# Kernel tuning notes

Hardware: AMD Instinct MI355X
Metric: run time of the kernel (lower is better)

The kernel has to match this reference:

```python
import jax, jax.numpy as jnp
import numpy as np

D_VOC, P_VOC, M_VOC = 2048, 1024, 4096
H = 256
T = 32
LD, LP, LM = 24, 12, 20


def _norm_adj(key, n):
    # binary graph + self loops, row-normalized (matches GCN.normalize(adj+I))
    a = (jax.random.uniform(key, (n, n)) < 0.002).astype(jnp.float32)
    a = a + jnp.eye(n, dtype=jnp.float32)
    rs = a.sum(axis=1)
    rinv = jnp.where(rs > 0, 1.0 / rs, 0.0)
    return rinv[:, None] * a


def setup_inputs() -> dict:
    key = jax.random.key(0)
    ks = jax.random.split(key, 32)
    s = float(1.0 / np.sqrt(H))
    u = lambda k, shape, sc: jax.random.uniform(k, shape, minval=-sc, maxval=sc, dtype=jnp.float32)
    inp = {
        'diag_codes': jax.random.randint(ks[0], (T, LD), 0, D_VOC),
        'proc_codes': jax.random.randint(ks[1], (T, LP), 0, P_VOC),
        'med_codes': jax.random.randint(ks[2], (T - 1, LM), 0, M_VOC),
        'diag_emb': u(ks[3], (D_VOC, H), 0.1),
        'proc_emb': u(ks[4], (P_VOC, H), 0.1),
        'gru_d_wih': u(ks[5], (3 * H, H), s), 'gru_d_whh': u(ks[6], (3 * H, H), s),
        'gru_d_bih': u(ks[7], (3 * H,), s), 'gru_d_bhh': u(ks[8], (3 * H,), s),
        'gru_p_wih': u(ks[9], (3 * H, H), s), 'gru_p_whh': u(ks[10], (3 * H, H), s),
        'gru_p_bih': u(ks[11], (3 * H,), s), 'gru_p_bhh': u(ks[12], (3 * H,), s),
        'q_w': u(ks[13], (2 * H, H), s), 'q_b': u(ks[14], (H,), s),
        'adj_ehr': _norm_adj(ks[15], M_VOC),
        'adj_ddi': _norm_adj(ks[16], M_VOC),
        'w1_ehr': u(ks[17], (M_VOC, H), s), 'b1_ehr': u(ks[18], (H,), s),
        'w2_ehr': u(ks[19], (H, H), s), 'b2_ehr': u(ks[20], (H,), s),
        'w1_ddi': u(ks[21], (M_VOC, H), s), 'b1_ddi': u(ks[22], (H,), s),
        'w2_ddi': u(ks[23], (H, H), s), 'b2_ddi': u(ks[24], (H,), s),
        'inter': jax.random.normal(ks[25], (1,), dtype=jnp.float32) / H,
        'proj_w': u(ks[26], (2 * H, H), s), 'proj_b': u(ks[27], (H,), s),
    }
    return inp


def _gru(x, wih, whh, bih, bhh):
    # torch.nn.GRU cell math; x: [T, H] -> outputs [T, H]
    def step(h, xt):
        gi = xt @ wih.T + bih
        gh = h @ whh.T + bhh
        ir, iz, inn = jnp.split(gi, 3)
        hr, hz, hn = jnp.split(gh, 3)
        r = jax.nn.sigmoid(ir + hr)
        z = jax.nn.sigmoid(iz + hz)
        n = jnp.tanh(inn + r * hn)
        h2 = (1.0 - z) * n + z * h
        return h2, h2
    _, ys = jax.lax.scan(step, jnp.zeros((x.shape[-1],), x.dtype), x)
    return ys


def _gcn(adj, w1, b1, w2, b2):
    # input features are identity, so first support mm(I, w1) == w1
    h1 = jax.nn.relu(adj @ w1 + b1)
    return adj @ (h1 @ w2) + b2


def reference(diag_codes, proc_codes, med_codes, diag_emb, proc_emb,
              gru_d_wih, gru_d_whh, gru_d_bih, gru_d_bhh,
              gru_p_wih, gru_p_whh, gru_p_bih, gru_p_bhh,
              q_w, q_b, adj_ehr, adj_ddi,
              w1_ehr, b1_ehr, w2_ehr, b2_ehr,
              w1_ddi, b1_ddi, w2_ddi, b2_ddi,
              inter, proj_w, proj_b):
    # ---- PatientEncoder: gather + sum codes per visit, GRU over visits ----
    seq_d = diag_emb[diag_codes].sum(axis=1)            # [T, H]
    seq_p = proc_emb[proc_codes].sum(axis=1)            # [T, H]
    od = _gru(seq_d, gru_d_wih, gru_d_whh, gru_d_bih, gru_d_bhh)
    op = _gru(seq_p, gru_p_wih, gru_p_whh, gru_p_bih, gru_p_bhh)
    feats = jnp.concatenate([od, op], axis=-1)          # [T, 2H]
    queries = jax.nn.relu(feats) @ q_w + q_b            # [T, H] (Sequential(ReLU, Linear))
    query = queries[-1:]                                # [1, H]
    history_keys = queries[:-1]                         # [T-1, H]
    # multi-hot history medication values (scatter)
    tm1 = med_codes.shape[0]
    history_values = jnp.zeros((tm1, M_VOC), jnp.float32).at[
        jnp.arange(tm1)[:, None], med_codes].set(1.0)   # [T-1, M_VOC]
    # ---- PriorEncoder ----
    prior = _gcn(adj_ehr, w1_ehr, b1_ehr, w2_ehr, b2_ehr) \
        - inter[0] * _gcn(adj_ddi, w1_ddi, b1_ddi, w2_ddi, b2_ddi)  # [M_VOC, H]
    w_emb = jax.nn.softmax(query @ prior.T, axis=-1)    # [1, M_VOC]
    # diag(w) @ prior == broadcast row-scale (the fused gather-weighted-scale)
    gc1 = w_emb.reshape(-1, 1) * prior                  # [M_VOC, H]
    visit_w = jax.nn.softmax(query @ history_keys.T, axis=-1)  # [1, T-1]
    wv = (visit_w @ history_values).reshape(-1, 1)      # [M_VOC, 1]
    gc2 = wv * prior                                    # [M_VOC, H]
    return jnp.concatenate([gc1, gc2], axis=-1) @ proj_w + proj_b  # [M_VOC, H]
```

## Files before the change

kernel.cpp:

```cpp
#include <hip/hip_runtime.h>
#include <hip/hip_bf16.h>

#define HD   256
#define TT   32
#define MV   4096
#define LD_  24
#define LP_  12
#define LM_  20
#define MAXNZ 96
#define SCAN_WPB 12

typedef _Float16 h2v __attribute__((ext_vector_type(2)));
typedef _Float16 h8  __attribute__((ext_vector_type(8)));

__device__ __forceinline__ float fdot2(h2v a, h2v b, float c) {
#if __has_builtin(__builtin_amdgcn_fdot2)
  return __builtin_amdgcn_fdot2(a, b, c, false);
#else
  return c + (float)a[0] * (float)b[0] + (float)a[1] * (float)b[1];
#endif
}

#define PIN2(x) { float _t = __builtin_bit_cast(float, x); \
                  asm volatile("" : "+v"(_t));             \
                  x = __builtin_bit_cast(h2v, _t); }

__global__ __launch_bounds__(768) void k0_cvt(
    const float* __restrict__ whh_d, const float* __restrict__ whh_p,
    h8* __restrict__ wt)
{
  const int i = blockIdx.x, b = blockIdx.y, g = threadIdx.x;
  const float* whh = b ? whh_p : whh_d;
  const float* src = whh + (size_t)g * HD + 8 * i;
  h8 v;
#pragma unroll
  for (int e = 0; e < 8; ++e) v[e] = (_Float16)src[e];
  wt[((size_t)b * 32 + i) * 768 + g] = v;
}

__global__ __launch_bounds__(768) void k1_embed_gi(
    const int* __restrict__ dc, const int* __restrict__ pc,
    const float* __restrict__ demb, const float* __restrict__ pemb,
    const float* __restrict__ wih_d, const float* __restrict__ bih_d,
    const float* __restrict__ wih_p, const float* __restrict__ bih_p,
    float* __restrict__ GI)
{
  const int t = blockIdx.x, b = blockIdx.y;
  const int* codes = b ? pc : dc;
  const int L = b ? LP_ : LD_;
  const float* emb = b ? pemb : demb;
  const float* wih = b ? wih_p : wih_d;
  const float* bih = b ? bih_p : bih_d;
  __shared__ float s[HD];
  const int j = threadIdx.x;
  if (j < HD) {
    float acc = 0.f;
    for (int l = 0; l < L; ++l) acc += emb[(size_t)codes[t * L + l] * HD + j];
    s[j] = acc;
  }
  __syncthreads();
  const int g = j;
  float acc = bih[g];
  const float* wr = wih + (size_t)g * HD;
  for (int k = 0; k < HD; k += 4) {
    float4 w4 = *(const float4*)(wr + k);
    acc = fmaf(w4.x, s[k], acc);
    acc = fmaf(w4.y, s[k + 1], acc);
    acc = fmaf(w4.z, s[k + 2], acc);
    acc = fmaf(w4.w, s[k + 3], acc);
  }
  GI[((size_t)b * TT + t) * 768 + g] = acc;
}

__global__ __launch_bounds__(768)
__attribute__((amdgpu_waves_per_eu(3, 3)))
void k23_fused(
    const float* __restrict__ GI, const h8* __restrict__ wt,
    const float* __restrict__ bhh_d, const float* __restrict__ bhh_p,
    float* __restrict__ feats,
    const float* __restrict__ adj_e, const float* __restrict__ adj_d,
    const float* __restrict__ w1_e, const float* __restrict__ b1_e,
    const float* __restrict__ w1_d, const float* __restrict__ b1_d,
    float* __restrict__ h1, int* __restrict__ cnt_g,
    int* __restrict__ cols_g, float* __restrict__ vals_g)
{
  __shared__ h8 hbuf[2][32];
  __shared__ float ghs[768];
  __shared__ int   scols[SCAN_WPB][MAXNZ];
  __shared__ float svals[SCAN_WPB][MAXNZ];

  if (blockIdx.x < 2) {
    const int b = blockIdx.x, g = threadIdx.x;
    const float* gi = GI + (size_t)b * TT * 768;
    const float* bhh = b ? bhh_p : bhh_d;

    h2v w[128];
    {
      const h8* wrow = wt + (size_t)b * 32 * 768 + g;
#pragma unroll
      for (int i = 0; i < 32; ++i) {
        union { h8 v; h2v p[4]; } u;
        u.v = wrow[(size_t)i * 768];
        w[4 * i + 0] = u.p[0];
        w[4 * i + 1] = u.p[1];
        w[4 * i + 2] = u.p[2];
        w[4 * i + 3] = u.p[3];
      }
    }
#pragma unroll
    for (int i = 0; i < 128; ++i) PIN2(w[i])

    const float bh = bhh[g];
    float hreg = 0.f;
    if (g < HD) ((_Float16*)&hbuf[0][0])[g] = (_Float16)0.f;
    __syncthreads();

    for (int t = 0; t < TT; ++t) {
      const float* git = gi + t * 768;
      float ir = 0.f, iz = 0.f, inn = 0.f;
      if (g < HD) { ir = git[g]; iz = git[HD + g]; inn = git[2 * HD + g]; }

      const h8* hb = hbuf[t & 1];
      float d0 = 0.f, d1 = 0.f, d2 = 0.f, d3 = 0.f;
#pragma unroll
      for (int i = 0; i < 32; ++i) {
        union { h8 v; h2v p[4]; } u;
        u.v = hb[i];
        d0 = fdot2(w[4 * i + 0], u.p[0], d0);
        d1 = fdot2(w[4 * i + 1], u.p[1], d1);
        d2 = fdot2(w[4 * i + 2], u.p[2], d2);
        d3 = fdot2(w[4 * i + 3], u.p[3], d3);
      }
      ghs[g] = (d0 + d1) + (d2 + d3) + bh;
      __syncthreads();
      if (g < HD) {
        const float hr = ghs[g], hz = ghs[HD + g], hn = ghs[2 * HD + g];
        const float r = 1.f / (1.f + __expf(-(ir + hr)));
        const float z = 1.f / (1.f + __expf(-(iz + hz)));
        const float n = tanhf(inn + r * hn);
        hreg = (1.f - z) * n + z * hreg;
        ((_Float16*)&hbuf[(t & 1) ^ 1][0])[g] = (_Float16)hreg;
        feats[(size_t)t * 512 + b * HD + g] = hreg;
      }
      __syncthreads();
    }
    return;
  }

  const int w = threadIdx.x >> 6, lane = threadIdx.x & 63;
  const int rg = (blockIdx.x - 2) * SCAN_WPB + w;
  if (rg >= 2 * MV) return;
  const int bsel = rg >> 12;
  const int r = rg & (MV - 1);
  const float* adj = (bsel ? adj_d : adj_e) + (size_t)r * MV;
  const float* w1 = bsel ? w1_d : w1_e;
  const float* b1 = bsel ? b1_d : b1_e;

  float4 ev[16];
#pragma unroll
  for (int c = 0; c < 16; ++c)
    ev[c] = *(const float4*)(adj + c * 256 + lane * 4);

  int cl = 0;
#pragma unroll
  for (int c = 0; c < 16; ++c)
    cl += (ev[c].x != 0.f) + (ev[c].y != 0.f) + (ev[c].z != 0.f) + (ev[c].w != 0.f);

  int pref = cl;
#pragma unroll
  for (int ofs = 1; ofs < 64; ofs <<= 1) {
    int v = __shfl_up(pref, ofs, 64);
    if (lane >= ofs) pref += v;
  }
  const int total = __shfl(pref, 63, 64);
  int pos = pref - cl;

#pragma unroll
  for (int c = 0; c < 16; ++c) {
    const float vv[4] = {ev[c].x, ev[c].y, ev[c].z, ev[c].w};
#pragma unroll
    for (int e = 0; e < 4; ++e) {
      if (vv[e] != 0.f) {
        if (pos < MAXNZ) {
          scols[w][pos] = c * 256 + lane * 4 + e;
          svals[w][pos] = vv[e];
        }
        ++pos;
      }
    }
  }
  const int n = total > MAXNZ ? MAXNZ : total;

  float4 acc = *(const float4*)(b1 + lane * 4);
  for (int k = 0; k < n; ++k) {
    const int col = scols[w][k];
    const float v = svals[w][k];
    const float4 wv4 = *(const float4*)(w1 + (size_t)col * HD + lane * 4);
    acc.x = fmaf(v, wv4.x, acc.x);
    acc.y = fmaf(v, wv4.y, acc.y);
    acc.z = fmaf(v, wv4.z, acc.z);
    acc.w = fmaf(v, wv4.w, acc.w);
  }
  float4 hro;
  hro.x = fmaxf(acc.x, 0.f); hro.y = fmaxf(acc.y, 0.f);
  hro.z = fmaxf(acc.z, 0.f); hro.w = fmaxf(acc.w, 0.f);
  *(float4*)(h1 + (size_t)rg * HD + lane * 4) = hro;

  if (lane == 0) cnt_g[rg] = n;
  for (int k = lane; k < n; k += 64) {
    cols_g[(size_t)rg * MAXNZ + k] = scols[w][k];
    vals_g[(size_t)rg * MAXNZ + k] = svals[w][k];
  }
}

__global__ __launch_bounds__(256) void k2b_queries(
    const float* __restrict__ feats, const float* __restrict__ q_w,
    const float* __restrict__ q_b, float* __restrict__ queries)
{
  const int t = blockIdx.x, j = threadIdx.x;
  __shared__ float f[512];
  f[j] = fmaxf(feats[(size_t)t * 512 + j], 0.f);
  f[j + 256] = fmaxf(feats[(size_t)t * 512 + 256 + j], 0.f);
  __syncthreads();
  float acc = q_b[j];
  for (int k = 0; k < 512; ++k) acc = fmaf(f[k], q_w[(size_t)k * HD + j], acc);
  queries[(size_t)t * HD + j] = acc;
}

__global__ __launch_bounds__(512) void k4_z(
    const float* __restrict__ h1, const float* __restrict__ w2_e,
    const float* __restrict__ w2_d, float* __restrict__ zz)
{
  const int blk = blockIdx.x, b = blockIdx.y;
  const int t = threadIdx.x;
  const int j = t & 255, half = t >> 8;
  const float* w2 = b ? w2_d : w2_e;
  const float* h1b = h1 + (size_t)b * MV * HD + (size_t)blk * 8 * HD;
  __shared__ float tile[8][HD];
  __shared__ float part[8][HD];
  {
    float4* t4 = (float4*)tile;
    const float4* s4 = (const float4*)h1b;
    t4[t] = s4[t];
  }
  __syncthreads();
  float acc[8];
#pragma unroll
  for (int r = 0; r < 8; ++r) acc[r] = 0.f;
  const int k0 = half * 128;
  for (int k = k0; k < k0 + 128; k += 4) {
    float wa = w2[(size_t)(k + 0) * HD + j];
    float wb = w2[(size_t)(k + 1) * HD + j];
    float wc = w2[(size_t)(k + 2) * HD + j];
    float wd = w2[(size_t)(k + 3) * HD + j];
#pragma unroll
    for (int r = 0; r < 8; ++r) {
      float4 tv = *(const float4*)&tile[r][k];
      acc[r] = fmaf(tv.x, wa, acc[r]);
      acc[r] = fmaf(tv.y, wb, acc[r]);
      acc[r] = fmaf(tv.z, wc, acc[r]);
      acc[r] = fmaf(tv.w, wd, acc[r]);
    }
  }
  if (half == 1) {
#pragma unroll
    for (int r = 0; r < 8; ++r) part[r][j] = acc[r];
  }
  __syncthreads();
  if (half == 0) {
    float* zb = zz + (size_t)b * MV * HD + (size_t)blk * 8 * HD;
#pragma unroll
    for (int r = 0; r < 8; ++r) zb[r * HD + j] = acc[r] + part[r][j];
  }
}

__global__ __launch_bounds__(256) void k5_prior(
    const float* __restrict__ zz, const int* __restrict__ cnt_g,
    const int* __restrict__ cols_g, const float* __restrict__ vals_g,
    const float* __restrict__ b2_e, const float* __restrict__ b2_d,
    const float* __restrict__ inter, const float* __restrict__ queries,
    float* __restrict__ prior, float* __restrict__ s1)
{
  const int r = blockIdx.x, j = threadIdx.x;
  __shared__ float red[256];
  float acc_e = b2_e[j];
  {
    const int ne = cnt_g[r];
    const int* ce = cols_g + (size_t)r * MAXNZ;
    const float* ve = vals_g + (size_t)r * MAXNZ;
    for (int k = 0; k < ne; ++k)
      acc_e = fmaf(ve[k], zz[(size_t)ce[k] * HD + j], acc_e);
  }
  float acc_d = b2_d[j];
  {
    const int nd = cnt_g[MV + r];
    const int* cd = cols_g + (size_t)(MV + r) * MAXNZ;
    const float* vd = vals_g + (size_t)(MV + r) * MAXNZ;
    const float* zd = zz + (size_t)MV * HD;
    for (int k = 0; k < nd; ++k)
      acc_d = fmaf(vd[k], zd[(size_t)cd[k] * HD + j], acc_d);
  }
  const float pr = acc_e - inter[0] * acc_d;
  prior[(size_t)r * HD + j] = pr;
  red[j] = queries[31 * HD + j] * pr;
  __syncthreads();
  for (int s = 128; s > 0; s >>= 1) {
    if (j < s) red[j] += red[j + s];
    __syncthreads();
  }
  if (j == 0) s1[r] = red[0];
}

__global__ __launch_bounds__(1024) void k6a_softmax(
    const float* __restrict__ s1, const float* __restrict__ queries,
    float* __restrict__ w_emb, float* __restrict__ visw)
{
  const int j = threadIdx.x;
  __shared__ float red[1024];
  __shared__ float s2[31];
  float m = -1e30f;
  for (int i = j; i < MV; i += 1024) m = fmaxf(m, s1[i]);
  red[j] = m;
  __syncthreads();
  for (int s = 512; s > 0; s >>= 1) {
    if (j < s) red[j] = fmaxf(red[j], red[j + s]);
    __syncthreads();
  }
  const float mx = red[0];
  __syncthreads();
  float sum = 0.f;
  for (int i = j; i < MV; i += 1024) sum += __expf(s1[i] - mx);
  red[j] = sum;
  __syncthreads();
  for (int s = 512; s > 0; s >>= 1) {
    if (j < s) red[j] += red[j + s];
    __syncthreads();
  }
  const float inv = 1.f / red[0];
  for (int i = j; i < MV; i += 1024) w_emb[i] = __expf(s1[i] - mx) * inv;

  if (j < 31) {
    float acc = 0.f;
    for (int k = 0; k < HD; ++k)
      acc = fmaf(queries[31 * HD + k], queries[(size_t)j * HD + k], acc);
    s2[j] = acc;
  }
  __syncthreads();
  if (j == 0) {
    float mm = -1e30f;
    for (int t = 0; t < 31; ++t) mm = fmaxf(mm, s2[t]);
    float ss = 0.f;
    for (int t = 0; t < 31; ++t) ss += __expf(s2[t] - mm);
    const float is = 1.f / ss;
    for (int t = 0; t < 31; ++t) visw[t] = __expf(s2[t] - mm) * is;
  }
}

__global__ __launch_bounds__(1024) void k6b_wv(
    const int* __restrict__ med, const float* __restrict__ visw,
    float* __restrict__ wv)
{
  __shared__ int mc[31 * LM_];
  __shared__ float vw[31];
  const int j = threadIdx.x;
  if (j < 31 * LM_) mc[j] = med[j];
  if (j < 31) vw[j] = visw[j];
  __syncthreads();
  const int m = blockIdx.x * 1024 + j;
  float acc = 0.f;
  for (int t = 0; t < 31; ++t) {
    bool found = false;
#pragma unroll
    for (int l = 0; l < LM_; ++l) found = found || (mc[t * LM_ + l] == m);
    if (found) acc += vw[t];
  }
  wv[m] = acc;
}

__global__ __launch_bounds__(512) void k7_out(
    const float* __restrict__ prior, const float* __restrict__ w_emb,
    const float* __restrict__ wv, const float* __restrict__ proj_w,
    const float* __restrict__ proj_b, float* __restrict__ out)
{
  const int blk = blockIdx.x;
  const int t = threadIdx.x;
  const int j = t & 255, half = t >> 8;
  const int r0 = blk * 8;
  __shared__ float tile[8][HD];
  __shared__ float part[8][HD];
  __shared__ float we[8], wvv[8];
  {
    float4* t4 = (float4*)tile;
    const float4* s4 = (const float4*)(prior + (size_t)r0 * HD);
    t4[t] = s4[t];
  }
  if (t < 8) { we[t] = w_emb[r0 + t]; wvv[t] = wv[r0 + t]; }
  __syncthreads();
  const float* wmat = proj_w + (size_t)half * HD * HD;
  float acc[8];
#pragma unroll
  for (int r = 0; r < 8; ++r) acc[r] = 0.f;
  for (int k = 0; k < HD; k += 4) {
    float wa = wmat[(size_t)(k + 0) * HD + j];
    float wb = wmat[(size_t)(k + 1) * HD + j];
    float wc = wmat[(size_t)(k + 2) * HD + j];
    float wd = wmat[(size_t)(k + 3) * HD + j];
#pragma unroll
    for (int r = 0; r < 8; ++r) {
      float4 tv = *(const float4*)&tile[r][k];
      acc[r] = fmaf(tv.x, wa, acc[r]);
      acc[r] = fmaf(tv.y, wb, acc[r]);
      acc[r] = fmaf(tv.z, wc, acc[r]);
      acc[r] = fmaf(tv.w, wd, acc[r]);
    }
  }
  if (half == 1) {
#pragma unroll
    for (int r = 0; r < 8; ++r) part[r][j] = acc[r];
  }
  __syncthreads();
  if (half == 0) {
    const float pb = proj_b[j];
#pragma unroll
    for (int r = 0; r < 8; ++r)
      out[(size_t)(r0 + r) * HD + j] = we[r] * acc[r] + wvv[r] * part[r][j] + pb;
  }
}

extern "C" void kernel_launch(void* const* d_in, const int* in_sizes, int n_in,
                              void* d_out, int out_size, void* d_ws, size_t ws_size,
                              hipStream_t stream) {
  const int* diag_codes = (const int*)d_in[0];
  const int* proc_codes = (const int*)d_in[1];
  const int* med_codes  = (const int*)d_in[2];
  const float* diag_emb = (const float*)d_in[3];
  const float* proc_emb = (const float*)d_in[4];
  const float* wih_d = (const float*)d_in[5];
  const float* whh_d = (const float*)d_in[6];
  const float* bih_d = (const float*)d_in[7];
  const float* bhh_d = (const float*)d_in[8];
  const float* wih_p = (const float*)d_in[9];
  const float* whh_p = (const float*)d_in[10];
  const float* bih_p = (const float*)d_in[11];
  const float* bhh_p = (const float*)d_in[12];
  const float* q_w = (const float*)d_in[13];
  const float* q_b = (const float*)d_in[14];
  const float* adj_ehr = (const float*)d_in[15];
  const float* adj_ddi = (const float*)d_in[16];
  const float* w1_ehr = (const float*)d_in[17];
  const float* b1_ehr = (const float*)d_in[18];
  const float* w2_ehr = (const float*)d_in[19];
  const float* b2_ehr = (const float*)d_in[20];
  const float* w1_ddi = (const float*)d_in[21];
  const float* b1_ddi = (const float*)d_in[22];
  const float* w2_ddi = (const float*)d_in[23];
  const float* b2_ddi = (const float*)d_in[24];
  const float* inter = (const float*)d_in[25];
  const float* proj_w = (const float*)d_in[26];
  const float* proj_b = (const float*)d_in[27];
  float* out = (float*)d_out;

  float* ws = (float*)d_ws;
  size_t off = 0;
  float* GI      = ws + off; off += 2 * TT * 768;
  float* feats   = ws + off; off += TT * 512;
  float* queries = ws + off; off += TT * HD;
  float* h1      = ws + off; off += 2 * (size_t)MV * HD;
  float* zz      = ws + off; off += 2 * (size_t)MV * HD;
  float* prior   = ws + off; off += (size_t)MV * HD;
  float* s1      = ws + off; off += MV;
  float* w_emb   = ws + off; off += MV;
  float* visw    = ws + off; off += 32;
  float* wv      = ws + off; off += MV;
  int*   cnt_g   = (int*)(ws + off); off += 2 * MV;
  int*   cols_g  = (int*)(ws + off); off += 2 * (size_t)MV * MAXNZ;
  float* vals_g  = ws + off; off += 2 * (size_t)MV * MAXNZ;
  h8*    wt      = (h8*)(ws + off); off += 2 * 32 * 768 * 4;
  (void)ws_size; (void)in_sizes; (void)n_in; (void)out_size;

  const int scan_blocks = (2 * MV + SCAN_WPB - 1) / SCAN_WPB;

  k0_cvt<<<dim3(32, 2), 768, 0, stream>>>(whh_d, whh_p, wt);
  k1_embed_gi<<<dim3(TT, 2), 768, 0, stream>>>(diag_codes, proc_codes, diag_emb,
      proc_emb, wih_d, bih_d, wih_p, bih_p, GI);
  k23_fused<<<2 + scan_blocks, 768, 0, stream>>>(GI, wt, bhh_d, bhh_p, feats,
      adj_ehr, adj_ddi, w1_ehr, b1_ehr, w1_ddi, b1_ddi,
      h1, cnt_g, cols_g, vals_g);
  k2b_queries<<<TT, 256, 0, stream>>>(feats, q_w, q_b, queries);
  k4_z<<<dim3(MV / 8, 2), 512, 0, stream>>>(h1, w2_ehr, w2_ddi, zz);
  k5_prior<<<MV, 256, 0, stream>>>(zz, cnt_g, cols_g, vals_g, b2_ehr, b2_ddi,
      inter, queries, prior, s1);
  k6a_softmax<<<1, 1024, 0, stream>>>(s1, queries, w_emb, visw);
  k6b_wv<<<MV / 1024, 1024, 0, stream>>>(med_codes, visw, wv);
  k7_out<<<MV / 8, 512, 0, stream>>>(prior, w_emb, wv, proj_w, proj_b, out);
}
```

Measured before the change: 196.8 us.

## Split GRU from adjacency scan and fuse sparse first GCN layer into z kernel

The fused kernel that overlapped the two serial GRU blocks with the adjacency scan is split into a standalone scan/extract kernel and a GRU-only kernel. The sparse first GCN layer (adj @ w1, relu) moves into the z kernel, which removes the h1 round-trip through global memory. GRU weights are now held in AGPRs via inline accvgpr write/read instead of pinned VGPRs. The cost is losing the overlap of the long serial GRU with the scan, since the two now run back to back on one stream.

```diff
diff --git a/kernel.cpp b/kernel.cpp
--- a/kernel.cpp
+++ b/kernel.cpp
@@ -8,7 +8,6 @@
 #define LP_  12
 #define LM_  20
 #define MAXNZ 96
-#define SCAN_WPB 12
 
 typedef _Float16 h2v __attribute__((ext_vector_type(2)));
 typedef _Float16 h8  __attribute__((ext_vector_type(8)));
@@ -20,10 +19,6 @@
   return c + (float)a[0] * (float)b[0] + (float)a[1] * (float)b[1];
 #endif
 }
-
-#define PIN2(x) { float _t = __builtin_bit_cast(float, x); \
-                  asm volatile("" : "+v"(_t));             \
-                  x = __builtin_bit_cast(h2v, _t); }
 
 __global__ __launch_bounds__(768) void k0_cvt(
     const float* __restrict__ whh_d, const float* __restrict__ whh_p,
@@ -74,142 +69,70 @@
 
 __global__ __launch_bounds__(768)
 __attribute__((amdgpu_waves_per_eu(3, 3)))
-void k23_fused(
+void k2_gru(
     const float* __restrict__ GI, const h8* __restrict__ wt,
     const float* __restrict__ bhh_d, const float* __restrict__ bhh_p,
-    float* __restrict__ feats,
-    const float* __restrict__ adj_e, const float* __restrict__ adj_d,
-    const float* __restrict__ w1_e, const float* __restrict__ b1_e,
-    const float* __restrict__ w1_d, const float* __restrict__ b1_d,
-    float* __restrict__ h1, int* __restrict__ cnt_g,
-    int* __restrict__ cols_g, float* __restrict__ vals_g)
-{
+    float* __restrict__ feats)
+{
+  const int b = blockIdx.x, g = threadIdx.x;
+  const float* gi = GI + (size_t)b * TT * 768;
+  const float* bhh = b ? bhh_p : bhh_d;
+
   __shared__ h8 hbuf[2][32];
   __shared__ float ghs[768];
-  __shared__ int   scols[SCAN_WPB][MAXNZ];
-  __shared__ float svals[SCAN_WPB][MAXNZ];
-
-  if (blockIdx.x < 2) {
-    const int b = blockIdx.x, g = threadIdx.x;
-    const float* gi = GI + (size_t)b * TT * 768;
-    const float* bhh = b ? bhh_p : bhh_d;
-
-    h2v w[128];
-    {
-      const h8* wrow = wt + (size_t)b * 32 * 768 + g;
-#pragma unroll
-      for (int i = 0; i < 32; ++i) {
-        union { h8 v; h2v p[4]; } u;
-        u.v = wrow[(size_t)i * 768];
-        w[4 * i + 0] = u.p[0];
-        w[4 * i + 1] = u.p[1];
-        w[4 * i + 2] = u.p[2];
-        w[4 * i + 3] = u.p[3];
-      }
-    }
-#pragma unroll
-    for (int i = 0; i < 128; ++i) PIN2(w[i])
-
-    const float bh = bhh[g];
-    float hreg = 0.f;
-    if (g < HD) ((_Float16*)&hbuf[0][0])[g] = (_Float16)0.f;
+
+  float wa[128];
+  {
+    const h8* wrow = wt + (size_t)b * 32 * 768 + g;
+#pragma unroll
+    for (int i = 0; i < 32; ++i) {
+      union { h8 v; float f[4]; } u;
+      u.v = wrow[(size_t)i * 768];
+#pragma unroll
+      for (int e = 0; e < 4; ++e)
+        asm volatile("v_accvgpr_write_b32 %0, %1"
+                     : "=a"(wa[4 * i + e]) : "v"(u.f[e]));
+    }
+  }
+
+  const float bh = bhh[g];
+  float hreg = 0.f;
+  if (g < HD) ((_Float16*)&hbuf[0][0])[g] = (_Float16)0.f;
+  __syncthreads();
+
+  for (int t = 0; t < TT; ++t) {
+    const float* git = gi + t * 768;
+    float ir = 0.f, iz = 0.f, inn = 0.f;
+    if (g < HD) { ir = git[g]; iz = git[HD + g]; inn = git[2 * HD + g]; }
+
+    const h8* hb = hbuf[t & 1];
+    float d0 = 0.f, d1 = 0.f, d2 = 0.f, d3 = 0.f;
+#pragma unroll
+    for (int i = 0; i < 32; ++i) {
+      union { h8 v; h2v p[4]; } u;
+      u.v = hb[i];
+      float w0, w1, w2, w3;
+      asm("v_accvgpr_read_b32 %0, %1" : "=v"(w0) : "a"(wa[4 * i + 0]));
+      asm("v_accvgpr_read_b32 %0, %1" : "=v"(w1) : "a"(wa[4 * i + 1]));
+      asm("v_accvgpr_read_b32 %0, %1" : "=v"(w2) : "a"(wa[4 * i + 2]));
+      asm("v_accvgpr_read_b32 %0, %1" : "=v"(w3) : "a"(wa[4 * i + 3]));
+      d0 = fdot2(__builtin_bit_cast(h2v, w0), u.p[0], d0);
+      d1 = fdot2(__builtin_bit_cast(h2v, w1), u.p[1], d1);
+      d2 = fdot2(__builtin_bit_cast(h2v, w2), u.p[2], d2);
+      d3 = fdot2(__builtin_bit_cast(h2v, w3), u.p[3], d3);
+    }
+    ghs[g] = (d0 + d1) + (d2 + d3) + bh;
     __syncthreads();
-
-    for (int t = 0; t < TT; ++t) {
-      const float* git = gi + t * 768;
-      float ir = 0.f, iz = 0.f, inn = 0.f;
-      if (g < HD) { ir = git[g]; iz = git[HD + g]; inn = git[2 * HD + g]; }
-
-      const h8* hb = hbuf[t & 1];
-      float d0 = 0.f, d1 = 0.f, d2 = 0.f, d3 = 0.f;
-#pragma unroll
-      for (int i = 0; i < 32; ++i) {
-        union { h8 v; h2v p[4]; } u;
-        u.v = hb[i];
-        d0 = fdot2(w[4 * i + 0], u.p[0], d0);
-        d1 = fdot2(w[4 * i + 1], u.p[1], d1);
-        d2 = fdot2(w[4 * i + 2], u.p[2], d2);
-        d3 = fdot2(w[4 * i + 3], u.p[3], d3);
-      }
-      ghs[g] = (d0 + d1) + (d2 + d3) + bh;
-      __syncthreads();
-      if (g < HD) {
-        const float hr = ghs[g], hz = ghs[HD + g], hn = ghs[2 * HD + g];
-        const float r = 1.f / (1.f + __expf(-(ir + hr)));
-        const float z = 1.f / (1.f + __expf(-(iz + hz)));
-        const float n = tanhf(inn + r * hn);
-        hreg = (1.f - z) * n + z * hreg;
-        ((_Float16*)&hbuf[(t & 1) ^ 1][0])[g] = (_Float16)hreg;
-        feats[(size_t)t * 512 + b * HD + g] = hreg;
-      }
-      __syncthreads();
-    }
-    return;
-  }
-
-  const int w = threadIdx.x >> 6, lane = threadIdx.x & 63;
-  const int rg = (blockIdx.x - 2) * SCAN_WPB + w;
-  if (rg >= 2 * MV) return;
-  const int bsel = rg >> 12;
-  const int r = rg & (MV - 1);
-  const float* adj = (bsel ? adj_d : adj_e) + (size_t)r * MV;
-  const float* w1 = bsel ? w1_d : w1_e;
-  const float* b1 = bsel ? b1_d : b1_e;
-
-  float4 ev[16];
-#pragma unroll
-  for (int c = 0; c < 16; ++c)
-    ev[c] = *(const float4*)(adj + c * 256 + lane * 4);
-
-  int cl = 0;
-#pragma unroll
-  for (int c = 0; c < 16; ++c)
-    cl += (ev[c].x != 0.f) + (ev[c].y != 0.f) + (ev[c].z != 0.f) + (ev[c].w != 0.f);
-
-  int pref = cl;
-#pragma unroll
-  for (int ofs = 1; ofs < 64; ofs <<= 1) {
-    int v = __shfl_up(pref, ofs, 64);
-    if (lane >= ofs) pref += v;
-  }
-  const int total = __shfl(pref, 63, 64);
-  int pos = pref - cl;
-
-#pragma unroll
-  for (int c = 0; c < 16; ++c) {
-    const float vv[4] = {ev[c].x, ev[c].y, ev[c].z, ev[c].w};
-#pragma unroll
-    for (int e = 0; e < 4; ++e) {
-      if (vv[e] != 0.f) {
-        if (pos < MAXNZ) {
-          scols[w][pos] = c * 256 + lane * 4 + e;
-          svals[w][pos] = vv[e];
-        }
-        ++pos;
-      }
-    }
-  }
-  const int n = total > MAXNZ ? MAXNZ : total;
-
-  float4 acc = *(const float4*)(b1 + lane * 4);
-  for (int k = 0; k < n; ++k) {
-    const int col = scols[w][k];
-    const float v = svals[w][k];
-    const float4 wv4 = *(const float4*)(w1 + (size_t)col * HD + lane * 4);
-    acc.x = fmaf(v, wv4.x, acc.x);
-    acc.y = fmaf(v, wv4.y, acc.y);
-    acc.z = fmaf(v, wv4.z, acc.z);
-    acc.w = fmaf(v, wv4.w, acc.w);
-  }
-  float4 hro;
-  hro.x = fmaxf(acc.x, 0.f); hro.y = fmaxf(acc.y, 0.f);
-  hro.z = fmaxf(acc.z, 0.f); hro.w = fmaxf(acc.w, 0.f);
-  *(float4*)(h1 + (size_t)rg * HD + lane * 4) = hro;
-
-  if (lane == 0) cnt_g[rg] = n;
-  for (int k = lane; k < n; k += 64) {
-    cols_g[(size_t)rg * MAXNZ + k] = scols[w][k];
-    vals_g[(size_t)rg * MAXNZ + k] = svals[w][k];
+    if (g < HD) {
+      const float hr = ghs[g], hz = ghs[HD + g], hn = ghs[2 * HD + g];
+      const float r = 1.f / (1.f + __expf(-(ir + hr)));
+      const float z = 1.f / (1.f + __expf(-(iz + hz)));
+      const float n = tanhf(inn + r * hn);
+      hreg = (1.f - z) * n + z * hreg;
+      ((_Float16*)&hbuf[(t & 1) ^ 1][0])[g] = (_Float16)hreg;
+      feats[(size_t)t * 512 + b * HD + g] = hreg;
+    }
+    __syncthreads();
   }
 }
 
@@ -227,23 +150,91 @@
   queries[(size_t)t * HD + j] = acc;
 }
 
-__global__ __launch_bounds__(512) void k4_z(
-    const float* __restrict__ h1, const float* __restrict__ w2_e,
-    const float* __restrict__ w2_d, float* __restrict__ zz)
+__global__ __launch_bounds__(256) void k3a_extract(
+    const float* __restrict__ adj_e, const float* __restrict__ adj_d,
+    int* __restrict__ cnt_g, int* __restrict__ cols_g,
+    float* __restrict__ vals_g)
+{
+  const int w = threadIdx.x >> 6, lane = threadIdx.x & 63;
+  const int rg = blockIdx.x * 4 + w;
+  const int bsel = rg >> 12;
+  const int r = rg & (MV - 1);
+  const float* adj = (bsel ? adj_d : adj_e) + (size_t)r * MV;
+
+  float4 ev[16];
+#pragma unroll
+  for (int c = 0; c < 16; ++c)
+    ev[c] = *(const float4*)(adj + c * 256 + lane * 4);
+
+  int cl = 0;
+#pragma unroll
+  for (int c = 0; c < 16; ++c)
+    cl += (ev[c].x != 0.f) + (ev[c].y != 0.f) + (ev[c].z != 0.f) + (ev[c].w != 0.f);
+
+  int pref = cl;
+#pragma unroll
+  for (int ofs = 1; ofs < 64; ofs <<= 1) {
+    int v = __shfl_up(pref, ofs, 64);
+    if (lane >= ofs) pref += v;
+  }
+  const int total = __shfl(pref, 63, 64);
+  int pos = pref - cl;
+
+  int* cg = cols_g + (size_t)rg * MAXNZ;
+  float* vg = vals_g + (size_t)rg * MAXNZ;
+#pragma unroll
+  for (int c = 0; c < 16; ++c) {
+    const float vv[4] = {ev[c].x, ev[c].y, ev[c].z, ev[c].w};
+#pragma unroll
+    for (int e = 0; e < 4; ++e) {
+      if (vv[e] != 0.f) {
+        if (pos < MAXNZ) { cg[pos] = c * 256 + lane * 4 + e; vg[pos] = vv[e]; }
+        ++pos;
+      }
+    }
+  }
+  if (lane == 0) cnt_g[rg] = total > MAXNZ ? MAXNZ : total;
+}
+
+__global__ __launch_bounds__(512) void k45_z(
+    const int* __restrict__ cnt_g, const int* __restrict__ cols_g,
+    const float* __restrict__ vals_g,
+    const float* __restrict__ w1_e, const float* __restrict__ b1_e,
+    const float* __restrict__ w1_d, const float* __restrict__ b1_d,
+    const float* __restrict__ w2_e, const float* __restrict__ w2_d,
+    float* __restrict__ zz)
 {
   const int blk = blockIdx.x, b = blockIdx.y;
   const int t = threadIdx.x;
+  __shared__ float tile[8][HD];
+  __shared__ float part[8][HD];
+
+  {
+    const int w = t >> 6, lane = t & 63;
+    const int rg = b * MV + blk * 8 + w;
+    const float* w1 = b ? w1_d : w1_e;
+    const float* b1 = b ? b1_d : b1_e;
+    const int n = cnt_g[rg];
+    const int* cg = cols_g + (size_t)rg * MAXNZ;
+    const float* vg = vals_g + (size_t)rg * MAXNZ;
+    float4 acc = *(const float4*)(b1 + lane * 4);
+    for (int k = 0; k < n; ++k) {
+      const int col = cg[k];
+      const float v = vg[k];
+      const float4 wv4 = *(const float4*)(w1 + (size_t)col * HD + lane * 4);
+      acc.x = fmaf(v, wv4.x, acc.x);
+      acc.y = fmaf(v, wv4.y, acc.y);
+      acc.z = fmaf(v, wv4.z, acc.z);
+      acc.w = fmaf(v, wv4.w, acc.w);
+    }
+    float4* dst = (float4*)&tile[w][lane * 4];
+    dst->x = fmaxf(acc.x, 0.f); dst->y = fmaxf(acc.y, 0.f);
+    dst->z = fmaxf(acc.z, 0.f); dst->w = fmaxf(acc.w, 0.f);
+  }
+  __syncthreads();
+
   const int j = t & 255, half = t >> 8;
   const float* w2 = b ? w2_d : w2_e;
-  const float* h1b = h1 + (size_t)b * MV * HD + (size_t)blk * 8 * HD;
-  __shared__ float tile[8][HD];
-  __shared__ float part[8][HD];
-  {
-    float4* t4 = (float4*)tile;
-    const float4* s4 = (const float4*)h1b;
-    t4[t] = s4[t];
-  }
-  __syncthreads();
   float acc[8];
 #pragma unroll
   for (int r = 0; r < 8; ++r) acc[r] = 0.f;
@@ -465,7 +456,6 @@
   float* GI      = ws + off; off += 2 * TT * 768;
   float* feats   = ws + off; off += TT * 512;
   float* queries = ws + off; off += TT * HD;
-  float* h1      = ws + off; off += 2 * (size_t)MV * HD;
   float* zz      = ws + off; off += 2 * (size_t)MV * HD;
   float* prior   = ws + off; off += (size_t)MV * HD;
   float* s1      = ws + off; off += MV;
@@ -478,16 +468,15 @@
   h8*    wt      = (h8*)(ws + off); off += 2 * 32 * 768 * 4;
   (void)ws_size; (void)in_sizes; (void)n_in; (void)out_size;
 
-  const int scan_blocks = (2 * MV + SCAN_WPB - 1) / SCAN_WPB;
-
   k0_cvt<<<dim3(32, 2), 768, 0, stream>>>(whh_d, whh_p, wt);
   k1_embed_gi<<<dim3(TT, 2), 768, 0, stream>>>(diag_codes, proc_codes, diag_emb,
       proc_emb, wih_d, bih_d, wih_p, bih_p, GI);
-  k23_fused<<<2 + scan_blocks, 768, 0, stream>>>(GI, wt, bhh_d, bhh_p, feats,
-      adj_ehr, adj_ddi, w1_ehr, b1_ehr, w1_ddi, b1_ddi,
-      h1, cnt_g, cols_g, vals_g);
+  k3a_extract<<<2 * MV / 4, 256, 0, stream>>>(adj_ehr, adj_ddi,
+      cnt_g, cols_g, vals_g);
+  k2_gru<<<2, 768, 0, stream>>>(GI, wt, bhh_d, bhh_p, feats);
   k2b_queries<<<TT, 256, 0, stream>>>(feats, q_w, q_b, queries);
-  k4_z<<<dim3(MV / 8, 2), 512, 0, stream>>>(h1, w2_ehr, w2_ddi, zz);
+  k45_z<<<dim3(MV / 8, 2), 512, 0, stream>>>(cnt_g, cols_g, vals_g,
+      w1_ehr, b1_ehr, w1_ddi, b1_ddi, w2_ehr, w2_ddi, zz);
   k5_prior<<<MV, 256, 0, stream>>>(zz, cnt_g, cols_g, vals_g, b2_ehr, b2_ddi,
       inter, queries, prior, s1);
   k6a_softmax<<<1, 1024, 0, stream>>>(s1, queries, w_emb, visw);
```

New measurement: 257.2 us. 30.7% more time.
